# Kernel tuning notes

Hardware: AMD Instinct MI355X
Metric: run time of the kernel (lower is better)

## Reference

```python
import jax, jax.numpy as jnp
import numpy as np

B, CH, D, H, W = 8, 64, 32, 64, 64
S = CH // 2  # shrink


def setup_inputs() -> dict:
    key = jax.random.key(0)
    ks = jax.random.split(key, 10)
    sc = 0.05
    x = jax.random.normal(ks[0], (B, CH, D, H, W), jnp.float32)
    Wk = jax.random.normal(ks[1], (S, CH), jnp.float32) * sc
    bk = jax.random.normal(ks[2], (S,), jnp.float32) * sc
    Wq = jax.random.normal(ks[3], (S, CH), jnp.float32) * sc
    bq = jax.random.normal(ks[4], (S,), jnp.float32) * sc
    Wv = jax.random.normal(ks[5], (S, CH), jnp.float32) * sc
    bv = jax.random.normal(ks[6], (S,), jnp.float32) * sc
    Wo = jax.random.normal(ks[7], (CH, S), jnp.float32) * sc
    bo = jax.random.normal(ks[8], (CH,), jnp.float32) * sc
    # original inits atten_factor to 0 (which zeroes the attention branch);
    # use a nonzero value so the attention path is exercised.
    factor = jnp.full((1,), 0.5, jnp.float32)
    return {"x": x, "Wk": Wk, "bk": bk, "Wq": Wq, "bq": bq,
            "Wv": Wv, "bv": bv, "Wo": Wo, "bo": bo, "factor": factor}


def reference(x, Wk, bk, Wq, bq, Wv, bv, Wo, bo, factor):
    b, c, d, h, w = x.shape
    s = Wk.shape[0]

    def proj(Wm, bm):
        # conv3d 1x1 + permute(0,3,4,1,2) fused: [B,C,D,H,W] -> [B,H,W,S,D]
        y = jnp.einsum('oc,bcdhw->bhwod', Wm, x) + bm[None, None, None, :, None]
        return y.reshape(b * h * w, s, d)

    k = proj(Wk, bk)
    q = proj(Wq, bq)
    v = proj(Wv, bv)
    # scores [N, D, D]; softmax over dim=1 (the k-derived axis), matching torch
    scores = jnp.einsum('nsi,nsj->nij', k, q) / jnp.sqrt(jnp.float32(s))
    a = jax.nn.softmax(scores, axis=1)
    o = jnp.einsum('nsd,ndj->nsj', v, a)                    # [N, S, D]
    o = o.reshape(b, h, w, s, d)
    # output conv1x1 back to C channels, layout [B,C,D,H,W]
    o = jnp.einsum('os,bhwsd->bodhw', Wo, o) + bo[None, :, None, None, None]
    y = x + factor[0] * o
    return jnp.mean(y, axis=2)                              # [B, C, H, W]
```

## Files before the change

### kernel.cpp

```cpp
#include <hip/hip_runtime.h>


namespace {
constexpr int kB = 8, kC = 64, kD = 32, kH = 64, kW = 64, kS = 32;
constexpr int kHW = kH * kW;
constexpr int TW = 16, NT = 512;

typedef unsigned short u16t;
typedef unsigned int u32t;
typedef __attribute__((ext_vector_type(8))) short bf16x8;
typedef __attribute__((ext_vector_type(4))) float f32x4;

#if defined(__has_builtin)
#if __has_builtin(__builtin_amdgcn_cvt_pk_bf16_f32)
#define HAS_CVT_PK_BF16 1
#endif
#endif

__device__ __forceinline__ u32t pack2(float lo, float hi) {
#ifdef HAS_CVT_PK_BF16
    typedef __attribute__((ext_vector_type(2))) __bf16 v2bf;
    union { v2bf v; u32t u; } cv;
    cv.v = __builtin_amdgcn_cvt_pk_bf16_f32(lo, hi);
    return cv.u;
#else
    union { u32t i; float f; } a, b;
    a.f = lo; b.f = hi;
    u32t ra = a.i + 0x7FFFu + ((a.i >> 16) & 1u);
    u32t rb = b.i + 0x7FFFu + ((b.i >> 16) & 1u);
    return (ra >> 16) | (rb & 0xFFFF0000u);
#endif
}
__device__ __forceinline__ bf16x8 pack8(const float4 f0, const float4 f1) {
    union { bf16x8 v; u32t u[4]; } r;
    r.u[0] = pack2(f0.x, f0.y); r.u[1] = pack2(f0.z, f0.w);
    r.u[2] = pack2(f1.x, f1.y); r.u[3] = pack2(f1.z, f1.w);
    return r.v;
}
__device__ __forceinline__ float bsel(u32t q, int odd) {
    union { u32t i; float f; } v;
    v.i = odd ? (q & 0xFFFF0000u) : (q << 16);
    return v.f;
}
}

__global__ __launch_bounds__(NT, 4) void attn_fused(
    const float* __restrict__ x,
    const float* __restrict__ Wk, const float* __restrict__ bk,
    const float* __restrict__ Wq, const float* __restrict__ bq,
    const float* __restrict__ Wv, const float* __restrict__ bv,
    const float* __restrict__ Wo, const float* __restrict__ bo,
    const float* __restrict__ factor,
    float* __restrict__ out)
{
    __shared__ __align__(16) u16t KQX[512 * 64];
    __shared__ u32t XbP[4 * 512];
    __shared__ float AbarS[16 * kD];
    __shared__ __align__(16) float ObarS[16 * 36];

    const int t = threadIdx.x;
    const int lane = t & 63;
    const int wv = t >> 6;
    const int l15 = lane & 15;
    const int quad = lane >> 4;

    const int blk = blockIdx.x;
    const int bh = (blk & 7) | ((blk >> 5) << 3);
    const int wt = (blk >> 3) & 3;
    const int b = bh >> 6, h = bh & 63, w0 = wt * TW;

    {
        const float* xb = x + (size_t)(b * kC * kD) * kHW + h * kW + w0;
        const int w4 = t & 3, cp = (t >> 2) & 31, dv = t >> 7;
        const float* p0 = xb + (size_t)((cp * 2) * kD + dv) * kHW + w4 * 4;
        const float* p1 = p0 + (size_t)kD * kHW;
        float4 fa[8], fb[8];
        #pragma unroll
        for (int it = 0; it < 8; ++it) {
            fa[it] = *(const float4*)(p0 + (size_t)(it * 4) * kHW);
            fb[it] = *(const float4*)(p1 + (size_t)(it * 4) * kHW);
        }
        __builtin_amdgcn_sched_barrier(0);
        asm volatile("" ::
            "v"(fa[0].x), "v"(fa[1].x), "v"(fa[2].x), "v"(fa[3].x),
            "v"(fa[4].x), "v"(fa[5].x), "v"(fa[6].x), "v"(fa[7].x),
            "v"(fb[0].x), "v"(fb[1].x), "v"(fb[2].x), "v"(fb[3].x),
            "v"(fb[4].x), "v"(fb[5].x), "v"(fb[6].x), "v"(fb[7].x));

        float4 sA = fa[0], sB = fb[0];
        #pragma unroll
        for (int it = 1; it < 8; ++it) {
            sA.x += fa[it].x; sA.y += fa[it].y; sA.z += fa[it].z; sA.w += fa[it].w;
            sB.x += fb[it].x; sB.y += fb[it].y; sB.z += fb[it].z; sB.w += fb[it].w;
        }
        {
            const int wbase = dv * 512 + w4 * 128;
            XbP[wbase + 0 * 32 + (cp ^ (w4 * 4 + 0))] = pack2(sA.x, sB.x);
            XbP[wbase + 1 * 32 + (cp ^ (w4 * 4 + 1))] = pack2(sA.y, sB.y);
            XbP[wbase + 2 * 32 + (cp ^ (w4 * 4 + 2))] = pack2(sA.z, sB.z);
            XbP[wbase + 3 * 32 + (cp ^ (w4 * 4 + 3))] = pack2(sA.w, sB.w);
        }

        u32t* dst = (u32t*)KQX;
        const int gsw = cp >> 2, gin = cp & 3;
        #pragma unroll
        for (int it = 0; it < 8; ++it) {
            int d = dv + it * 4;
            int sw = d & 7;
            int pg = ((gsw ^ sw) ^ (w4 << 1)) * 4 + gin;
            int r0 = w4 * 128 + d;
            dst[(r0 + 0 * 32) * 32 + pg] = pack2(fa[it].x, fb[it].x);
            dst[(r0 + 1 * 32) * 32 + pg] = pack2(fa[it].y, fb[it].y);
            dst[(r0 + 2 * 32) * 32 + pg] = pack2(fa[it].z, fb[it].z);
            dst[(r0 + 3 * 32) * 32 + pg] = pack2(fa[it].w, fb[it].w);
        }
    }

    bf16x8 Af[3][2][2];
    float4 bias4[3][2];
    {
        const float* Wp[3] = {Wk, Wq, Wv};
        const float* bp[3] = {bk, bq, bv};
        #pragma unroll
        for (int p = 0; p < 3; ++p) {
            #pragma unroll
            for (int m0 = 0; m0 < 2; ++m0) {
                #pragma unroll
                for (int ks = 0; ks < 2; ++ks) {
                    const float* src = Wp[p] + (m0 * 16 + l15) * kC + ks * 32 + quad * 8;
                    Af[p][m0][ks] = pack8(*(const float4*)src, *(const float4*)(src + 4));
                }
                bias4[p][m0] = *(const float4*)(bp[p] + m0 * 16 + quad * 4);
            }
        }
    }
    __syncthreads();

    bf16x8 Bf[4][2];
    #pragma unroll
    for (int nt = 0; nt < 4; ++nt) {
        int row = wv * 64 + nt * 16 + l15;
        int gx = (row & 7) ^ ((row >> 7) << 1);
        #pragma unroll
        for (int ks = 0; ks < 2; ++ks)
            Bf[nt][ks] = *(const bf16x8*)&KQX[row * 64 + ((ks * 4 + quad) ^ gx) * 8];
    }

    f32x4 Vf[2][4];
    #pragma unroll
    for (int p = 0; p < 3; ++p) {
        #pragma unroll
        for (int m0 = 0; m0 < 2; ++m0) {
            #pragma unroll
            for (int nt = 0; nt < 4; ++nt) {
                f32x4 acc = {0.f, 0.f, 0.f, 0.f};
                acc = __builtin_amdgcn_mfma_f32_16x16x32_bf16(Af[p][m0][0], Bf[nt][0], acc, 0, 0, 0);
                acc = __builtin_amdgcn_mfma_f32_16x16x32_bf16(Af[p][m0][1], Bf[nt][1], acc, 0, 0, 0);
                if (p < 2) {
                    u32t lo = pack2(acc[0] + bias4[p][m0].x, acc[1] + bias4[p][m0].y);
                    u32t hi = pack2(acc[2] + bias4[p][m0].z, acc[3] + bias4[p][m0].w);
                    int row = wv * 64 + nt * 16 + l15;
                    int gx = (row & 7) ^ ((row >> 7) << 1);
                    int g = (p == 0 ? 0 : 4) + m0 * 2 + (quad >> 1);
                    uint2 pr; pr.x = lo; pr.y = hi;
                    *(uint2*)&KQX[row * 64 + ((g ^ gx) * 8) + (quad & 1) * 4] = pr;
                } else {
                    Vf[m0][nt][0] = acc[0] + bias4[2][m0].x;
                    Vf[m0][nt][1] = acc[1] + bias4[2][m0].y;
                    Vf[m0][nt][2] = acc[2] + bias4[2][m0].z;
                    Vf[m0][nt][3] = acc[3] + bias4[2][m0].w;
                }
            }
        }
    }

    {
        const float kScaleLog2e = 0.25501700249569946f;
        #pragma unroll
        for (int si = 0; si < 2; ++si) {
            int wp = wv * 2 + si;
            bf16x8 Ka[2], Qb[2];
            #pragma unroll
            for (int m0 = 0; m0 < 2; ++m0) {
                int rr = wp * 32 + m0 * 16 + l15;
                int gx = (rr & 7) ^ ((rr >> 7) << 1);
                Ka[m0] = *(const bf16x8*)&KQX[rr * 64 + ((quad ^ gx) * 8)];
            }
            #pragma unroll
            for (int n0 = 0; n0 < 2; ++n0) {
                int rr = wp * 32 + n0 * 16 + l15;
                int gx = (rr & 7) ^ ((rr >> 7) << 1);
                Qb[n0] = *(const bf16x8*)&KQX[rr * 64 + (((4 + quad) ^ gx) * 8)];
            }
            f32x4 sc[2][2];
            #pragma unroll
            for (int m0 = 0; m0 < 2; ++m0)
                #pragma unroll
                for (int n0 = 0; n0 < 2; ++n0) {
                    f32x4 z = {0.f, 0.f, 0.f, 0.f};
                    sc[m0][n0] = __builtin_amdgcn_mfma_f32_16x16x32_bf16(Ka[m0], Qb[n0], z, 0, 0, 0);
                }
            #pragma unroll
            for (int n0 = 0; n0 < 2; ++n0) {
                float sum = 0.f;
                #pragma unroll
                for (int m0 = 0; m0 < 2; ++m0)
                    #pragma unroll
                    for (int r2 = 0; r2 < 4; ++r2) {
                        float e = exp2f(sc[m0][n0][r2] * kScaleLog2e);
                        sc[m0][n0][r2] = e; sum += e;
                    }
                sum += __shfl_xor(sum, 16);
                sum += __shfl_xor(sum, 32);
                float inv = __builtin_amdgcn_rcpf(sum);
                #pragma unroll
                for (int m0 = 0; m0 < 2; ++m0)
                    #pragma unroll
                    for (int r2 = 0; r2 < 4; ++r2) sc[m0][n0][r2] *= inv;
            }
            #pragma unroll
            for (int m0 = 0; m0 < 2; ++m0)
                #pragma unroll
                for (int r2 = 0; r2 < 4; ++r2) {
                    float v2 = sc[m0][0][r2] + sc[m0][1][r2];
                    v2 += __shfl_xor(v2, 1);
                    v2 += __shfl_xor(v2, 2);
                    v2 += __shfl_xor(v2, 4);
                    v2 += __shfl_xor(v2, 8);
                    if (l15 == 0)
                        AbarS[wp * kD + m0 * 16 + quad * 4 + r2] = v2 * (1.0f / kD);
                }
            {
                float ab0 = AbarS[wp * kD + l15];
                float ab1 = AbarS[wp * kD + 16 + l15];
                #pragma unroll
                for (int m0 = 0; m0 < 2; ++m0)
                    #pragma unroll
                    for (int r2 = 0; r2 < 4; ++r2) {
                        float v = Vf[m0][2 * si + 0][r2] * ab0
                                + Vf[m0][2 * si + 1][r2] * ab1;
                        v += __shfl_xor(v, 1);
                        v += __shfl_xor(v, 2);
                        v += __shfl_xor(v, 4);
                        v += __shfl_xor(v, 8);
                        if (l15 == 0)
                            ObarS[wp * 36 + m0 * 16 + quad * 4 + r2] = v;
                    }
            }
        }
    }
    __syncthreads();

    {
        const float fac = factor[0];
        const int wp = t & 15, cl = t >> 4;
        const float4* obp = (const float4*)&ObarS[wp * 36];
        float4 ob4[8];
        #pragma unroll
        for (int s4 = 0; s4 < 8; ++s4) ob4[s4] = obp[s4];
        const int odd = cl & 1;
        #pragma unroll
        for (int half = 0; half < 2; ++half) {
            int c = cl + half * 32;
            int cpi = (cl >> 1) + half * 16;
            const int xi = wp * 32 + (cpi ^ wp);
            float xbar = bsel(XbP[0 * 512 + xi], odd)
                       + bsel(XbP[1 * 512 + xi], odd)
                       + bsel(XbP[2 * 512 + xi], odd)
                       + bsel(XbP[3 * 512 + xi], odd);
            xbar *= (1.0f / kD);
            const float4* wrow = (const float4*)(Wo + c * kS);
            float acc = 0.f;
            #pragma unroll
            for (int s4 = 0; s4 < 8; ++s4) {
                float4 w4 = wrow[s4];
                acc += w4.x * ob4[s4].x;
                acc += w4.y * ob4[s4].y;
                acc += w4.z * ob4[s4].z;
                acc += w4.w * ob4[s4].w;
            }
            out[((b * kC + c) * kH + h) * kW + w0 + wp] =
                xbar + fac * (bo[c] + acc);
        }
    }
}

extern "C" void kernel_launch(void* const* d_in, const int* in_sizes, int n_in,
                              void* d_out, int out_size, void* d_ws, size_t ws_size,
                              hipStream_t stream) {
    const float* x      = (const float*)d_in[0];
    const float* Wk     = (const float*)d_in[1];
    const float* bk     = (const float*)d_in[2];
    const float* Wq     = (const float*)d_in[3];
    const float* bq     = (const float*)d_in[4];
    const float* Wv     = (const float*)d_in[5];
    const float* bv     = (const float*)d_in[6];
    const float* Wo     = (const float*)d_in[7];
    const float* bo     = (const float*)d_in[8];
    const float* factor = (const float*)d_in[9];
    float* out = (float*)d_out;

    dim3 grid(kB * kH * (kW / TW));
    attn_fused<<<grid, NT, 0, stream>>>(x, Wk, bk, Wq, bq, Wv, bv, Wo, bo, factor, out);
}
```

Baseline: 419.5 us.

## Process two W-tiles per block with prefetch of second tile during softmax

Each block now handles two consecutive 16-wide W tiles, which halves the grid. The global loads for the second tile are issued before and during the first tile's softmax, so memory latency overlaps with compute. Weights are reloaded through an asm barrier so the compiler does not keep them live across the tile boundary and inflate register use. In exchange there are half as many blocks to hide latency, extra register pressure from the prefetched float4 arrays, and an added block barrier.

```diff
diff --git a/kernel.cpp b/kernel.cpp
--- a/kernel.cpp
+++ b/kernel.cpp
@@ -65,28 +65,39 @@
     const int quad = lane >> 4;
 
     const int blk = blockIdx.x;
-    const int bh = (blk & 7) | ((blk >> 5) << 3);
-    const int wt = (blk >> 3) & 3;
-    const int b = bh >> 6, h = bh & 63, w0 = wt * TW;
-
-    {
-        const float* xb = x + (size_t)(b * kC * kD) * kHW + h * kW + w0;
-        const int w4 = t & 3, cp = (t >> 2) & 31, dv = t >> 7;
-        const float* p0 = xb + (size_t)((cp * 2) * kD + dv) * kHW + w4 * 4;
-        const float* p1 = p0 + (size_t)kD * kHW;
-        float4 fa[8], fb[8];
-        #pragma unroll
-        for (int it = 0; it < 8; ++it) {
-            fa[it] = *(const float4*)(p0 + (size_t)(it * 4) * kHW);
-            fb[it] = *(const float4*)(p1 + (size_t)(it * 4) * kHW);
-        }
-        __builtin_amdgcn_sched_barrier(0);
-        asm volatile("" ::
-            "v"(fa[0].x), "v"(fa[1].x), "v"(fa[2].x), "v"(fa[3].x),
-            "v"(fa[4].x), "v"(fa[5].x), "v"(fa[6].x), "v"(fa[7].x),
-            "v"(fb[0].x), "v"(fb[1].x), "v"(fb[2].x), "v"(fb[3].x),
-            "v"(fb[4].x), "v"(fb[5].x), "v"(fb[6].x), "v"(fb[7].x));
-
+    const int bh  = (blk & 7) | ((blk >> 4) << 3);
+    const int g   = (blk >> 3) & 1;
+    const int b = bh >> 6, h = bh & 63;
+    const int w0 = g * 32;
+
+    const int w4 = t & 3, cp = (t >> 2) & 31, dv = t >> 7;
+    const float* xb = x + (size_t)(b * kC * kD) * kHW + h * kW + w0;
+    const float* p0 = xb + (size_t)((cp * 2) * kD + dv) * kHW + w4 * 4;
+    const float* p1 = p0 + (size_t)kD * kHW;
+
+    bf16x8 Af[3][2][2];
+    float4 bias4[3][2];
+
+    auto load_weights = [&](const float* wkp, const float* bkp,
+                            const float* wqp, const float* bqp,
+                            const float* wvp, const float* bvp) {
+        const float* Wp[3] = {wkp, wqp, wvp};
+        const float* bp[3] = {bkp, bqp, bvp};
+        #pragma unroll
+        for (int p = 0; p < 3; ++p) {
+            #pragma unroll
+            for (int m0 = 0; m0 < 2; ++m0) {
+                #pragma unroll
+                for (int ks = 0; ks < 2; ++ks) {
+                    const float* src = Wp[p] + (m0 * 16 + l15) * kC + ks * 32 + quad * 8;
+                    Af[p][m0][ks] = pack8(*(const float4*)src, *(const float4*)(src + 4));
+                }
+                bias4[p][m0] = *(const float4*)(bp[p] + m0 * 16 + quad * 4);
+            }
+        }
+    };
+
+    auto stage_pack = [&](const float4 (&fa)[8], const float4 (&fb)[8]) {
         float4 sA = fa[0], sB = fb[0];
         #pragma unroll
         for (int it = 1; it < 8; ++it) {
@@ -100,7 +111,6 @@
             XbP[wbase + 2 * 32 + (cp ^ (w4 * 4 + 2))] = pack2(sA.z, sB.z);
             XbP[wbase + 3 * 32 + (cp ^ (w4 * 4 + 3))] = pack2(sA.w, sB.w);
         }
-
         u32t* dst = (u32t*)KQX;
         const int gsw = cp >> 2, gin = cp & 3;
         #pragma unroll
@@ -114,144 +124,120 @@
             dst[(r0 + 2 * 32) * 32 + pg] = pack2(fa[it].z, fb[it].z);
             dst[(r0 + 3 * 32) * 32 + pg] = pack2(fa[it].w, fb[it].w);
         }
-    }
-
-    bf16x8 Af[3][2][2];
-    float4 bias4[3][2];
-    {
-        const float* Wp[3] = {Wk, Wq, Wv};
-        const float* bp[3] = {bk, bq, bv};
+    };
+
+    auto do_proj = [&](f32x4 (&Vf)[2][4]) {
+        bf16x8 Bf[4][2];
+        #pragma unroll
+        for (int nt = 0; nt < 4; ++nt) {
+            int row = wv * 64 + nt * 16 + l15;
+            int gx = (row & 7) ^ ((row >> 7) << 1);
+            #pragma unroll
+            for (int ks = 0; ks < 2; ++ks)
+                Bf[nt][ks] = *(const bf16x8*)&KQX[row * 64 + ((ks * 4 + quad) ^ gx) * 8];
+        }
         #pragma unroll
         for (int p = 0; p < 3; ++p) {
             #pragma unroll
             for (int m0 = 0; m0 < 2; ++m0) {
                 #pragma unroll
-                for (int ks = 0; ks < 2; ++ks) {
-                    const float* src = Wp[p] + (m0 * 16 + l15) * kC + ks * 32 + quad * 8;
-                    Af[p][m0][ks] = pack8(*(const float4*)src, *(const float4*)(src + 4));
+                for (int nt = 0; nt < 4; ++nt) {
+                    f32x4 acc = {0.f, 0.f, 0.f, 0.f};
+                    acc = __builtin_amdgcn_mfma_f32_16x16x32_bf16(Af[p][m0][0], Bf[nt][0], acc, 0, 0, 0);
+                    acc = __builtin_amdgcn_mfma_f32_16x16x32_bf16(Af[p][m0][1], Bf[nt][1], acc, 0, 0, 0);
+                    if (p < 2) {
+                        u32t lo = pack2(acc[0] + bias4[p][m0].x, acc[1] + bias4[p][m0].y);
+                        u32t hi = pack2(acc[2] + bias4[p][m0].z, acc[3] + bias4[p][m0].w);
+                        int row = wv * 64 + nt * 16 + l15;
+                        int gx = (row & 7) ^ ((row >> 7) << 1);
+                        int gq = (p == 0 ? 0 : 4) + m0 * 2 + (quad >> 1);
+                        uint2 pr; pr.x = lo; pr.y = hi;
+                        *(uint2*)&KQX[row * 64 + ((gq ^ gx) * 8) + (quad & 1) * 4] = pr;
+                    } else {
+                        Vf[m0][nt][0] = acc[0] + bias4[2][m0].x;
+                        Vf[m0][nt][1] = acc[1] + bias4[2][m0].y;
+                        Vf[m0][nt][2] = acc[2] + bias4[2][m0].z;
+                        Vf[m0][nt][3] = acc[3] + bias4[2][m0].w;
+                    }
                 }
-                bias4[p][m0] = *(const float4*)(bp[p] + m0 * 16 + quad * 4);
-            }
-        }
-    }
-    __syncthreads();
-
-    bf16x8 Bf[4][2];
-    #pragma unroll
-    for (int nt = 0; nt < 4; ++nt) {
-        int row = wv * 64 + nt * 16 + l15;
-        int gx = (row & 7) ^ ((row >> 7) << 1);
-        #pragma unroll
-        for (int ks = 0; ks < 2; ++ks)
-            Bf[nt][ks] = *(const bf16x8*)&KQX[row * 64 + ((ks * 4 + quad) ^ gx) * 8];
-    }
-
-    f32x4 Vf[2][4];
-    #pragma unroll
-    for (int p = 0; p < 3; ++p) {
+            }
+        }
+    };
+
+    const float kScaleLog2e = 0.25501700249569946f;
+    auto softmax_site = [&](int si, const f32x4 (&Vf)[2][4]) {
+        int wp = wv * 2 + si;
+        bf16x8 Ka[2], Qb[2];
         #pragma unroll
         for (int m0 = 0; m0 < 2; ++m0) {
-            #pragma unroll
-            for (int nt = 0; nt < 4; ++nt) {
-                f32x4 acc = {0.f, 0.f, 0.f, 0.f};
-                acc = __builtin_amdgcn_mfma_f32_16x16x32_bf16(Af[p][m0][0], Bf[nt][0], acc, 0, 0, 0);
-                acc = __builtin_amdgcn_mfma_f32_16x16x32_bf16(Af[p][m0][1], Bf[nt][1], acc, 0, 0, 0);
-                if (p < 2) {
-                    u32t lo = pack2(acc[0] + bias4[p][m0].x, acc[1] + bias4[p][m0].y);
-                    u32t hi = pack2(acc[2] + bias4[p][m0].z, acc[3] + bias4[p][m0].w);
-                    int row = wv * 64 + nt * 16 + l15;
-                    int gx = (row & 7) ^ ((row >> 7) << 1);
-                    int g = (p == 0 ? 0 : 4) + m0 * 2 + (quad >> 1);
-                    uint2 pr; pr.x = lo; pr.y = hi;
-                    *(uint2*)&KQX[row * 64 + ((g ^ gx) * 8) + (quad & 1) * 4] = pr;
-                } else {
-                    Vf[m0][nt][0] = acc[0] + bias4[2][m0].x;
-                    Vf[m0][nt][1] = acc[1] + bias4[2][m0].y;
-                    Vf[m0][nt][2] = acc[2] + bias4[2][m0].z;
-                    Vf[m0][nt][3] = acc[3] + bias4[2][m0].w;
+            int rr = wp * 32 + m0 * 16 + l15;
+            int gx = (rr & 7) ^ ((rr >> 7) << 1);
+            Ka[m0] = *(const bf16x8*)&KQX[rr * 64 + ((quad ^ gx) * 8)];
+        }
+        #pragma unroll
+        for (int n0 = 0; n0 < 2; ++n0) {
+            int rr = wp * 32 + n0 * 16 + l15;
+            int gx = (rr & 7) ^ ((rr >> 7) << 1);
+            Qb[n0] = *(const bf16x8*)&KQX[rr * 64 + (((4 + quad) ^ gx) * 8)];
+        }
+        f32x4 sc[2][2];
+        #pragma unroll
+        for (int m0 = 0; m0 < 2; ++m0)
+            #pragma unroll
+            for (int n0 = 0; n0 < 2; ++n0) {
+                f32x4 z = {0.f, 0.f, 0.f, 0.f};
+                sc[m0][n0] = __builtin_amdgcn_mfma_f32_16x16x32_bf16(Ka[m0], Qb[n0], z, 0, 0, 0);
+            }
+        #pragma unroll
+        for (int n0 = 0; n0 < 2; ++n0) {
+            float sum = 0.f;
+            #pragma unroll
+            for (int m0 = 0; m0 < 2; ++m0)
+                #pragma unroll
+                for (int r2 = 0; r2 < 4; ++r2) {
+                    float e = exp2f(sc[m0][n0][r2] * kScaleLog2e);
+                    sc[m0][n0][r2] = e; sum += e;
                 }
-            }
-        }
-    }
-
-    {
-        const float kScaleLog2e = 0.25501700249569946f;
-        #pragma unroll
-        for (int si = 0; si < 2; ++si) {
-            int wp = wv * 2 + si;
-            bf16x8 Ka[2], Qb[2];
-            #pragma unroll
-            for (int m0 = 0; m0 < 2; ++m0) {
-                int rr = wp * 32 + m0 * 16 + l15;
-                int gx = (rr & 7) ^ ((rr >> 7) << 1);
-                Ka[m0] = *(const bf16x8*)&KQX[rr * 64 + ((quad ^ gx) * 8)];
-            }
-            #pragma unroll
-            for (int n0 = 0; n0 < 2; ++n0) {
-                int rr = wp * 32 + n0 * 16 + l15;
-                int gx = (rr & 7) ^ ((rr >> 7) << 1);
-                Qb[n0] = *(const bf16x8*)&KQX[rr * 64 + (((4 + quad) ^ gx) * 8)];
-            }
-            f32x4 sc[2][2];
+            sum += __shfl_xor(sum, 16);
+            sum += __shfl_xor(sum, 32);
+            float inv = __builtin_amdgcn_rcpf(sum);
             #pragma unroll
             for (int m0 = 0; m0 < 2; ++m0)
                 #pragma unroll
-                for (int n0 = 0; n0 < 2; ++n0) {
-                    f32x4 z = {0.f, 0.f, 0.f, 0.f};
-                    sc[m0][n0] = __builtin_amdgcn_mfma_f32_16x16x32_bf16(Ka[m0], Qb[n0], z, 0, 0, 0);
+                for (int r2 = 0; r2 < 4; ++r2) sc[m0][n0][r2] *= inv;
+        }
+        #pragma unroll
+        for (int m0 = 0; m0 < 2; ++m0)
+            #pragma unroll
+            for (int r2 = 0; r2 < 4; ++r2) {
+                float v2 = sc[m0][0][r2] + sc[m0][1][r2];
+                v2 += __shfl_xor(v2, 1);
+                v2 += __shfl_xor(v2, 2);
+                v2 += __shfl_xor(v2, 4);
+                v2 += __shfl_xor(v2, 8);
+                if (l15 == 0)
+                    AbarS[wp * kD + m0 * 16 + quad * 4 + r2] = v2 * (1.0f / kD);
+            }
+        {
+            float ab0 = AbarS[wp * kD + l15];
+            float ab1 = AbarS[wp * kD + 16 + l15];
+            #pragma unroll
+            for (int m0 = 0; m0 < 2; ++m0)
+                #pragma unroll
+                for (int r2 = 0; r2 < 4; ++r2) {
+                    float v = Vf[m0][2 * si + 0][r2] * ab0
+                            + Vf[m0][2 * si + 1][r2] * ab1;
+                    v += __shfl_xor(v, 1);
+                    v += __shfl_xor(v, 2);
+                    v += __shfl_xor(v, 4);
+                    v += __shfl_xor(v, 8);
+                    if (l15 == 0)
+                        ObarS[wp * 36 + m0 * 16 + quad * 4 + r2] = v;
                 }
-            #pragma unroll
-            for (int n0 = 0; n0 < 2; ++n0) {
-                float sum = 0.f;
-                #pragma unroll
-                for (int m0 = 0; m0 < 2; ++m0)
-                    #pragma unroll
-                    for (int r2 = 0; r2 < 4; ++r2) {
-                        float e = exp2f(sc[m0][n0][r2] * kScaleLog2e);
-                        sc[m0][n0][r2] = e; sum += e;
-                    }
-                sum += __shfl_xor(sum, 16);
-                sum += __shfl_xor(sum, 32);
-                float inv = __builtin_amdgcn_rcpf(sum);
-                #pragma unroll
-                for (int m0 = 0; m0 < 2; ++m0)
-                    #pragma unroll
-                    for (int r2 = 0; r2 < 4; ++r2) sc[m0][n0][r2] *= inv;
-            }
-            #pragma unroll
-            for (int m0 = 0; m0 < 2; ++m0)
-                #pragma unroll
-                for (int r2 = 0; r2 < 4; ++r2) {
-                    float v2 = sc[m0][0][r2] + sc[m0][1][r2];
-                    v2 += __shfl_xor(v2, 1);
-                    v2 += __shfl_xor(v2, 2);
-                    v2 += __shfl_xor(v2, 4);
-                    v2 += __shfl_xor(v2, 8);
-                    if (l15 == 0)
-                        AbarS[wp * kD + m0 * 16 + quad * 4 + r2] = v2 * (1.0f / kD);
-                }
-            {
-                float ab0 = AbarS[wp * kD + l15];
-                float ab1 = AbarS[wp * kD + 16 + l15];
-                #pragma unroll
-                for (int m0 = 0; m0 < 2; ++m0)
-                    #pragma unroll
-                    for (int r2 = 0; r2 < 4; ++r2) {
-                        float v = Vf[m0][2 * si + 0][r2] * ab0
-                                + Vf[m0][2 * si + 1][r2] * ab1;
-                        v += __shfl_xor(v, 1);
-                        v += __shfl_xor(v, 2);
-                        v += __shfl_xor(v, 4);
-                        v += __shfl_xor(v, 8);
-                        if (l15 == 0)
-                            ObarS[wp * 36 + m0 * 16 + quad * 4 + r2] = v;
-                    }
-            }
-        }
-    }
-    __syncthreads();
-
-    {
+        }
+    };
+
+    auto do_epilogue = [&](int w0t) {
         const float fac = factor[0];
         const int wp = t & 15, cl = t >> 4;
         const float4* obp = (const float4*)&ObarS[wp * 36];
@@ -273,16 +259,61 @@
             float acc = 0.f;
             #pragma unroll
             for (int s4 = 0; s4 < 8; ++s4) {
-                float4 w4 = wrow[s4];
-                acc += w4.x * ob4[s4].x;
-                acc += w4.y * ob4[s4].y;
-                acc += w4.z * ob4[s4].z;
-                acc += w4.w * ob4[s4].w;
-            }
-            out[((b * kC + c) * kH + h) * kW + w0 + wp] =
+                float4 w4v = wrow[s4];
+                acc += w4v.x * ob4[s4].x;
+                acc += w4v.y * ob4[s4].y;
+                acc += w4v.z * ob4[s4].z;
+                acc += w4v.w * ob4[s4].w;
+            }
+            out[((b * kC + c) * kH + h) * kW + w0t + wp] =
                 xbar + fac * (bo[c] + acc);
         }
+    };
+
+    float4 fa[8], fb[8];
+    #pragma unroll
+    for (int it = 0; it < 8; ++it) {
+        fa[it] = *(const float4*)(p0 + (size_t)(it * 4) * kHW);
+        fb[it] = *(const float4*)(p1 + (size_t)(it * 4) * kHW);
     }
+    __builtin_amdgcn_sched_barrier(0);
+    stage_pack(fa, fb);
+    load_weights(Wk, bk, Wq, bq, Wv, bv);
+    __syncthreads();
+    f32x4 Vf[2][4];
+    do_proj(Vf);
+
+    float4 ga[8], gb[8];
+    #pragma unroll
+    for (int it = 0; it < 8; ++it)
+        ga[it] = *(const float4*)(p0 + (size_t)(it * 4) * kHW + 16);
+    __builtin_amdgcn_sched_barrier(0);
+    softmax_site(0, Vf);
+    #pragma unroll
+    for (int it = 0; it < 8; ++it)
+        gb[it] = *(const float4*)(p1 + (size_t)(it * 4) * kHW + 16);
+    __builtin_amdgcn_sched_barrier(0);
+    softmax_site(1, Vf);
+    __syncthreads();
+    do_epilogue(w0);
+    __syncthreads();
+
+    stage_pack(ga, gb);
+    {
+        unsigned long long uk = (unsigned long long)Wk, ubk = (unsigned long long)bk;
+        unsigned long long uq = (unsigned long long)Wq, ubq = (unsigned long long)bq;
+        unsigned long long uv = (unsigned long long)Wv, ubv = (unsigned long long)bv;
+        asm volatile("" : "+s"(uk), "+s"(ubk), "+s"(uq), "+s"(ubq), "+s"(uv), "+s"(ubv));
+        load_weights((const float*)uk, (const float*)ubk,
+                     (const float*)uq, (const float*)ubq,
+                     (const float*)uv, (const float*)ubv);
+    }
+    __syncthreads();
+    do_proj(Vf);
+    softmax_site(0, Vf);
+    softmax_site(1, Vf);
+    __syncthreads();
+    do_epilogue(w0 + 16);
 }
 
 extern "C" void kernel_launch(void* const* d_in, const int* in_sizes, int n_in,
@@ -300,6 +331,6 @@
     const float* factor = (const float*)d_in[9];
     float* out = (float*)d_out;
 
-    dim3 grid(kB * kH * (kW / TW));
+    dim3 grid(kB * kH * 2);
     attn_fused<<<grid, NT, 0, stream>>>(x, Wk, bk, Wq, bq, Wv, bv, Wo, bo, factor, out);
 }
```

Result: slower. 508.3 us (+21.1%).
